# Performance work log

Hardware: AMD Instinct MI355X
Metric: run time of the kernel (lower is better)

The kernel has to match this reference:

```python
import jax, jax.numpy as jnp
import numpy as np

D_NUM = 4      # domain_num
N_ES = 2       # n_expert_specific per domain
N_SH = 4       # total shared experts (n_expert_shared_list = [1,1,1,1])
DIN = 512      # input_dims
H = 256        # expert_params dims[-1]
B = 16384      # batch
NEG_INF = -jnp.inf


def setup_inputs() -> dict:
    key = jax.random.key(0)
    ks = jax.random.split(key, 10)
    s = 1.0 / np.sqrt(DIN)
    x_list = jax.random.normal(ks[0], (D_NUM + 1, B, DIN), jnp.float32)
    sim_domain = jax.random.randint(ks[1], (D_NUM, 2), 0, D_NUM, jnp.int32)
    W_spec = jax.random.normal(ks[2], (D_NUM, N_ES, DIN, H), jnp.float32) * s
    b_spec = jax.random.normal(ks[3], (D_NUM, N_ES, H), jnp.float32) * 0.01
    W_sh = jax.random.normal(ks[4], (N_SH, DIN, H), jnp.float32) * s
    b_sh = jax.random.normal(ks[5], (N_SH, H), jnp.float32) * 0.01
    W_gate = jax.random.normal(ks[6], (D_NUM, DIN, N_ES + N_SH), jnp.float32) * s
    b_gate = jax.random.normal(ks[7], (D_NUM, N_ES + N_SH), jnp.float32) * 0.01
    W_gate_sh = jax.random.normal(ks[8], (DIN, D_NUM * N_ES + N_SH), jnp.float32) * s
    b_gate_sh = jax.random.normal(ks[9], (D_NUM * N_ES + N_SH,), jnp.float32) * 0.01
    return {"x_list": x_list, "sim_domain": sim_domain, "W_spec": W_spec,
            "b_spec": b_spec, "W_sh": W_sh, "b_sh": b_sh, "W_gate": W_gate,
            "b_gate": b_gate, "W_gate_sh": W_gate_sh, "b_gate_sh": b_gate_sh}


def reference(x_list, sim_domain, W_spec, b_spec, W_sh, b_sh, W_gate, b_gate, W_gate_sh, b_gate_sh):
    xd = x_list[:D_NUM]          # [D, B, DIN] per-domain inputs
    xs = x_list[-1]              # [B, DIN] shared input
    # expert MLPs (single hidden layer, relu, dropout=0/eval)
    spec = jax.nn.relu(jnp.einsum('nbd,nedh->nbeh', xd, W_spec) + b_spec[:, None])  # [D,B,E,H]
    shared = jax.nn.relu(jnp.einsum('bd,edh->beh', xs, W_sh) + b_sh)                # [B,S,H]
    # specific gates: softmax activation inside MLP
    g = jax.nn.softmax(jnp.einsum('nbd,nde->nbe', xd, W_gate) + b_gate[:, None], axis=-1)  # [D,B,E+S]
    # mask shared experts of non-similar domains (expert_ranges[d] = [N_ES + d])
    mem = (sim_domain[:, :, None] == jnp.arange(D_NUM)[None, None, :]).any(axis=1)  # [D,D]
    mask = jnp.concatenate([jnp.zeros((D_NUM, N_ES), jnp.float32),
                            jnp.where(mem, 0.0, NEG_INF)], axis=1)                  # [D,E+S]
    # torch code re-softmaxes the (already softmaxed) gate after adding -inf mask
    g = jax.nn.softmax(g + mask[:, None, :], axis=-1)
    # weighted combine without materializing broadcasted shared experts
    outs = (jnp.einsum('nbe,nbeh->nbh', g[..., :N_ES], spec)
            + jnp.einsum('nbe,beh->nbh', g[..., N_ES:], shared))                    # [D,B,H]
    # shared gate (cur_level < n_level)
    gs = jax.nn.softmax(xs @ W_gate_sh + b_gate_sh, axis=-1)                         # [B,D*E+S]
    all_spec = spec.transpose(1, 0, 2, 3).reshape(spec.shape[1], D_NUM * N_ES, H)    # [B,D*E,H]
    out_sh = (jnp.einsum('be,beh->bh', gs[:, :D_NUM * N_ES], all_spec)
              + jnp.einsum('be,beh->bh', gs[:, D_NUM * N_ES:], shared))             # [B,H]
    return jnp.concatenate([outs, out_sh[None]], axis=0)                             # [D+1,B,H]
```

## Files before the change

### kernel.cpp

```cpp
#include <hip/hip_runtime.h>
#include <cstdint>
#include <cstddef>

#define D_NUM 4
#define N_ES  2
#define N_SH  4
#define DIN   512
#define HDIM  256
#define BB    16384
#define MHALF 8192
#define NMAT  12
#define NGATE 36

typedef __bf16 bf16x8 __attribute__((ext_vector_type(8)));
typedef float  f32x4  __attribute__((ext_vector_type(4)));

__device__ __forceinline__ unsigned short f2bf(float f) {
    union { float f; unsigned u; } v; v.f = f;
    unsigned u = v.u;
    unsigned r = (u + 0x7FFFu + ((u >> 16) & 1u)) >> 16;
    return (unsigned short)r;
}
__device__ __forceinline__ float bf2f(unsigned short u) {
    union { unsigned u; float f; } v; v.u = ((unsigned)u) << 16; return v.f;
}
__device__ __forceinline__ void async16(void* l, const void* g) {
    __builtin_amdgcn_global_load_lds(
        (const __attribute__((address_space(1))) void*)g,
        (__attribute__((address_space(3))) void*)l,
        16, 0, 0);
}

template<int CTRL, int RMASK>
__device__ __forceinline__ float dpp_sum_step(float v) {
    union { float f; int i; } a, b;
    a.f = v;
    b.i = __builtin_amdgcn_update_dpp(0, a.i, CTRL, RMASK, 0xF, true);
    return v + b.f;
}
__device__ __forceinline__ float wave_sum63(float v) {
    v = dpp_sum_step<0x111, 0xF>(v);
    v = dpp_sum_step<0x112, 0xF>(v);
    v = dpp_sum_step<0x114, 0xF>(v);
    v = dpp_sum_step<0x118, 0xF>(v);
    v = dpp_sum_step<0x142, 0xA>(v);
    v = dpp_sum_step<0x143, 0xC>(v);
    return v;
}

__global__ __launch_bounds__(256) void k_wconv(
    const float* __restrict__ Wspec,
    const float* __restrict__ Wsh,
    unsigned short* __restrict__ WT)
{
    __shared__ unsigned short t[64][65];
    const int mat = blockIdx.z;
    const int k0  = blockIdx.x * 64;
    const int h0  = blockIdx.y * 64;
    const float* src = (mat < 8) ? (Wspec + (size_t)mat * DIN * HDIM)
                                 : (Wsh   + (size_t)(mat - 8) * DIN * HDIM);
    #pragma unroll
    for (int i = 0; i < 16; ++i) {
        int idx = i * 256 + threadIdx.x;
        int r = idx >> 6, c = idx & 63;
        t[r][c] = f2bf(src[(size_t)(k0 + r) * HDIM + h0 + c]);
    }
    __syncthreads();
    #pragma unroll
    for (int i = 0; i < 16; ++i) {
        int idx = i * 256 + threadIdx.x;
        int r = idx >> 6, c = idx & 63;
        WT[(size_t)mat * HDIM * DIN + (size_t)(h0 + r) * DIN + k0 + c] = t[c][r];
    }
}

__global__ __launch_bounds__(256) void k_gwt(
    const float* __restrict__ Wg,
    const float* __restrict__ Wgs,
    float* __restrict__ WgT,
    float* __restrict__ WgsT)
{
    int i = blockIdx.x * 256 + threadIdx.x;
    if (i < 4 * 6 * 512) {
        int n = i / 3072, rem = i % 3072;
        int e = rem >> 9, k = rem & 511;
        WgT[i] = Wg[((size_t)n * DIN + k) * 6 + e];
    }
    if (i < 12 * 512) {
        int e = i >> 9, k = i & 511;
        WgsT[i] = Wgs[(size_t)k * 12 + e];
    }
}

__global__ __launch_bounds__(128) void k_prep(
    const float* __restrict__ x,
    const int*   __restrict__ simdom,
    const float* __restrict__ WgT,
    const float* __restrict__ bg,
    const float* __restrict__ WgsT,
    const float* __restrict__ bgs,
    unsigned short* __restrict__ xbf,
    float* __restrict__ gates)
{
    __shared__ float lgate[2][2][36];
    __shared__ float gsm[2][72];
    const int wave = threadIdx.x >> 6;
    const int lane = threadIdx.x & 63;
    const int row0 = blockIdx.x * 4 + wave * 2;
    const int k0   = lane * 8;

    float4 a0[5], b0[5], a1[5], b1[5];
    #pragma unroll
    for (int m = 0; m < 5; ++m) {
        const float* xp0 = x + ((size_t)m * BB + row0) * DIN + k0;
        a0[m] = ((const float4*)xp0)[0];
        b0[m] = ((const float4*)xp0)[1];
        const float* xp1 = xp0 + DIN;
        a1[m] = ((const float4*)xp1)[0];
        b1[m] = ((const float4*)xp1)[1];
    }
    __builtin_amdgcn_sched_barrier(0);

    #pragma unroll
    for (int m = 0; m < 5; ++m) {
        unsigned short* xbp = xbf + ((size_t)m * BB + row0) * DIN + k0;
        {
            union { unsigned short us[8]; uint4 v; } q0, q1;
            q0.us[0]=f2bf(a0[m].x); q0.us[1]=f2bf(a0[m].y);
            q0.us[2]=f2bf(a0[m].z); q0.us[3]=f2bf(a0[m].w);
            q0.us[4]=f2bf(b0[m].x); q0.us[5]=f2bf(b0[m].y);
            q0.us[6]=f2bf(b0[m].z); q0.us[7]=f2bf(b0[m].w);
            q1.us[0]=f2bf(a1[m].x); q1.us[1]=f2bf(a1[m].y);
            q1.us[2]=f2bf(a1[m].z); q1.us[3]=f2bf(a1[m].w);
            q1.us[4]=f2bf(b1[m].x); q1.us[5]=f2bf(b1[m].y);
            q1.us[6]=f2bf(b1[m].z); q1.us[7]=f2bf(b1[m].w);
            *(uint4*)xbp         = q0.v;
            *(uint4*)(xbp + DIN) = q1.v;
        }
        if (m < 4) {
            float z0[6], z1[6];
            #pragma unroll
            for (int e = 0; e < 6; ++e) {
                const float* wp = WgT + ((size_t)(m * 6 + e)) * DIN + k0;
                float4 wa = ((const float4*)wp)[0], wb = ((const float4*)wp)[1];
                z0[e] = a0[m].x*wa.x + a0[m].y*wa.y + a0[m].z*wa.z + a0[m].w*wa.w
                      + b0[m].x*wb.x + b0[m].y*wb.y + b0[m].z*wb.z + b0[m].w*wb.w;
                z1[e] = a1[m].x*wa.x + a1[m].y*wa.y + a1[m].z*wa.z + a1[m].w*wa.w
                      + b1[m].x*wb.x + b1[m].y*wb.y + b1[m].z*wb.z + b1[m].w*wb.w;
            }
            #pragma unroll
            for (int e = 0; e < 6; ++e) { z0[e] = wave_sum63(z0[e]); z1[e] = wave_sum63(z1[e]); }
            if (lane == 63) {
                #pragma unroll
                for (int e = 0; e < 6; ++e) {
                    lgate[wave][0][m * 6 + e] = z0[e];
                    lgate[wave][1][m * 6 + e] = z1[e];
                }
            }
        } else {
            float z0[12], z1[12];
            #pragma unroll
            for (int e = 0; e < 12; ++e) {
                const float* wp = WgsT + (size_t)e * DIN + k0;
                float4 wa = ((const float4*)wp)[0], wb = ((const float4*)wp)[1];
                z0[e] = a0[m].x*wa.x + a0[m].y*wa.y + a0[m].z*wa.z + a0[m].w*wa.w
                      + b0[m].x*wb.x + b0[m].y*wb.y + b0[m].z*wb.z + b0[m].w*wb.w;
                z1[e] = a1[m].x*wa.x + a1[m].y*wa.y + a1[m].z*wa.z + a1[m].w*wa.w
                      + b1[m].x*wb.x + b1[m].y*wb.y + b1[m].z*wb.z + b1[m].w*wb.w;
            }
            #pragma unroll
            for (int e = 0; e < 12; ++e) { z0[e] = wave_sum63(z0[e]); z1[e] = wave_sum63(z1[e]); }
            if (lane == 63) {
                #pragma unroll
                for (int e = 0; e < 12; ++e) {
                    lgate[wave][0][24 + e] = z0[e];
                    lgate[wave][1][24 + e] = z1[e];
                }
            }
        }
    }
    asm volatile("s_waitcnt lgkmcnt(0)" ::: "memory");
    __builtin_amdgcn_wave_barrier();

    if (lane < 2) {
        const float* lg = lgate[wave][lane];
        float*       go = &gsm[wave][lane * 36];
        #pragma unroll
        for (int n = 0; n < 4; ++n) {
            float z[6];
            #pragma unroll
            for (int e = 0; e < 6; ++e) z[e] = lg[n * 6 + e] + bg[n * 6 + e];
            float mx = z[0];
            #pragma unroll
            for (int e = 1; e < 6; ++e) mx = fmaxf(mx, z[e]);
            float sum = 0.f;
            #pragma unroll
            for (int e = 0; e < 6; ++e) { z[e] = __expf(z[e] - mx); sum += z[e]; }
            float inv = 1.f / sum;
            #pragma unroll
            for (int e = 0; e < 6; ++e) z[e] *= inv;
            int s0 = simdom[n * 2], s1 = simdom[n * 2 + 1];
            float w[6];
            w[0] = z[0]; w[1] = z[1];
            #pragma unroll
            for (int j = 0; j < 4; ++j)
                w[2 + j] = (s0 == j || s1 == j) ? z[2 + j] : -1e30f;
            float mx2 = w[0];
            #pragma unroll
            for (int e = 1; e < 6; ++e) mx2 = fmaxf(mx2, w[e]);
            float sm = 0.f;
            #pragma unroll
            for (int e = 0; e < 6; ++e) { w[e] = __expf(w[e] - mx2); sm += w[e]; }
            float iv = 1.f / sm;
            #pragma unroll
            for (int e = 0; e < 6; ++e) go[n * 6 + e] = w[e] * iv;
        }
        {
            float z[12];
            #pragma unroll
            for (int e = 0; e < 12; ++e) z[e] = lg[24 + e] + bgs[e];
            float mx = z[0];
            #pragma unroll
            for (int e = 1; e < 12; ++e) mx = fmaxf(mx, z[e]);
            float sum = 0.f;
            #pragma unroll
            for (int e = 0; e < 12; ++e) { z[e] = __expf(z[e] - mx); sum += z[e]; }
            float inv = 1.f / sum;
            #pragma unroll
            for (int e = 0; e < 12; ++e) go[24 + e] = z[e] * inv;
        }
    }
    __builtin_amdgcn_wave_barrier();
    for (int j = lane; j < 72; j += 64)
        gates[(size_t)row0 * NGATE + j] = gsm[wave][j];
}

__global__ __launch_bounds__(256) void k_gemm(
    const unsigned short* __restrict__ xbf,
    const unsigned short* __restrict__ WT,
    const float* __restrict__ bspec,
    const float* __restrict__ bsh,
    unsigned short* __restrict__ S,
    int row_base)
{
    __shared__ unsigned short lbuf[17408];

    const int tid  = threadIdx.x;
    const int wave = tid >> 6;
    const int lane = tid & 63;

    const int j    = blockIdx.x + 24 * blockIdx.y;
    const int xcd  = j & 7;
    const int slot = j >> 3;
    const int rg   = xcd * 8 + slot / 24;
    const int mh   = slot % 24;

    const int mat  = mh >> 1;
    const int hh0  = (mh & 1) * 128;
    const int plane = (mat < 8) ? (mat >> 1) : 4;
    const int lrow0 = rg * 128;

    const unsigned short* Abase = xbf + ((size_t)plane * BB + row_base + lrow0) * DIN;
    const unsigned short* Bbase = WT + (size_t)mat * HDIM * DIN + (size_t)hh0 * DIN;

    const unsigned short* gb = (wave < 2) ? Abase : Bbase;
    unsigned goff[8];
    unsigned loff[8];
    {
        int cg = (lane & 7) ^ ((lane >> 3) & 7);
        #pragma unroll
        for (int i = 0; i < 8; ++i) {
            int slot2 = wave * 8 + i;
            int r = (slot2 & 15) * 8 + (lane >> 3);
            goff[i] = (unsigned)(r * DIN + cg * 8);
            loff[i] = (unsigned)(slot2 * 512);
        }
    }

    f32x4 acc[4][4];
    #pragma unroll
    for (int t = 0; t < 4; ++t)
        #pragma unroll
        for (int u = 0; u < 4; ++u)
            acc[t][u] = (f32x4){0.f, 0.f, 0.f, 0.f};

    const int wm = wave >> 1, wn = wave & 1;
    const int arow = lane & 15, quad = lane >> 4;
    int aofs[4], bofs[4];
    #pragma unroll
    for (int t = 0; t < 4; ++t) {
        int r = wm * 64 + t * 16 + arow;
        aofs[t] = r * 64 + (quad ^ (r & 7)) * 8;
    }
    #pragma unroll
    for (int u = 0; u < 4; ++u) {
        int r = wn * 64 + u * 16 + arow;
        bofs[u] = 8192 + r * 64 + (quad ^ (r & 7)) * 8;
    }

    for (int ks = 0; ks < 8; ++ks) {
        __syncthreads();
        #pragma unroll
        for (int i = 0; i < 8; ++i) {
            async16(lbuf + loff[i], gb + goff[i]);
            goff[i] += 64;
        }
        __syncthreads();

        #pragma unroll
        for (int s2 = 0; s2 < 2; ++s2) {
            const int sx = s2 * 32;
            bf16x8 af[4], bv[4];
            #pragma unroll
            for (int t = 0; t < 4; ++t) af[t] = *(const bf16x8*)(lbuf + (aofs[t] ^ sx));
            #pragma unroll
            for (int u = 0; u < 4; ++u) bv[u] = *(const bf16x8*)(lbuf + (bofs[u] ^ sx));
            #pragma unroll
            for (int t = 0; t < 4; ++t)
                #pragma unroll
                for (int u = 0; u < 4; ++u)
                    acc[t][u] = __builtin_amdgcn_mfma_f32_16x16x32_bf16(af[t], bv[u], acc[t][u], 0, 0, 0);
        }
    }

    __syncthreads();
    #pragma unroll
    for (int u = 0; u < 4; ++u) {
        const int hc = wn * 64 + u * 16 + arow;
        const float bias = (mat < 8) ? bspec[mat * HDIM + hh0 + hc]
                                     : bsh[(mat - 8) * HDIM + hh0 + hc];
        #pragma unroll
        for (int t = 0; t < 4; ++t) {
            const int rbase = wm * 64 + t * 16 + quad * 4;
            #pragma unroll
            for (int reg = 0; reg < 4; ++reg) {
                float v = fmaxf(acc[t][u][reg] + bias, 0.f);
                lbuf[(rbase + reg) * 136 + hc] = f2bf(v);
            }
        }
    }
    __syncthreads();
    {
        unsigned short* Sb = S + ((size_t)mat * MHALF + lrow0) * HDIM + hh0;
        #pragma unroll
        for (int i = 0; i < 8; ++i) {
            int idx = i * 256 + tid;
            int row = idx >> 4, c8 = idx & 15;
            *(uint4*)(Sb + (size_t)row * HDIM + c8 * 8) =
                *(const uint4*)(lbuf + row * 136 + c8 * 8);
        }
    }
}

__global__ __launch_bounds__(256) void k_comb(
    const unsigned short* __restrict__ S,
    const float* __restrict__ gates,
    float* __restrict__ out,
    int row_base)
{
    const int tid = threadIdx.x;
    const int h0  = (tid & 63) * 4;
    const int r0  = blockIdx.x * 8 + (tid >> 6) * 2;
    #pragma unroll
    for (int rr = 0; rr < 2; ++rr) {
        const int lr = r0 + rr;
        const int grow = row_base + lr;
        const float* g = gates + (size_t)grow * NGATE;
        float s[NMAT][4];
        #pragma unroll
        for (int mat = 0; mat < NMAT; ++mat) {
            uint2 u = *(const uint2*)(S + ((size_t)mat * MHALF + lr) * HDIM + h0);
            s[mat][0] = bf2f((unsigned short)(u.x & 0xFFFFu));
            s[mat][1] = bf2f((unsigned short)(u.x >> 16));
            s[mat][2] = bf2f((unsigned short)(u.y & 0xFFFFu));
            s[mat][3] = bf2f((unsigned short)(u.y >> 16));
        }
        float o4[4] = {0.f, 0.f, 0.f, 0.f};
        #pragma unroll
        for (int jj = 0; jj < 8; ++jj)
            #pragma unroll
            for (int c = 0; c < 4; ++c) o4[c] += g[24 + jj] * s[jj][c];
        #pragma unroll
        for (int e = 0; e < 4; ++e)
            #pragma unroll
            for (int c = 0; c < 4; ++c) o4[c] += g[32 + e] * s[8 + e][c];
        #pragma unroll
        for (int n = 0; n < 4; ++n) {
            float4 on;
            on.x = g[n*6+0]*s[n*2][0] + g[n*6+1]*s[n*2+1][0]
                 + g[n*6+2]*s[8][0] + g[n*6+3]*s[9][0] + g[n*6+4]*s[10][0] + g[n*6+5]*s[11][0];
            on.y = g[n*6+0]*s[n*2][1] + g[n*6+1]*s[n*2+1][1]
                 + g[n*6+2]*s[8][1] + g[n*6+3]*s[9][1] + g[n*6+4]*s[10][1] + g[n*6+5]*s[11][1];
            on.z = g[n*6+0]*s[n*2][2] + g[n*6+1]*s[n*2+1][2]
                 + g[n*6+2]*s[8][2] + g[n*6+3]*s[9][2] + g[n*6+4]*s[10][2] + g[n*6+5]*s[11][2];
            on.w = g[n*6+0]*s[n*2][3] + g[n*6+1]*s[n*2+1][3]
                 + g[n*6+2]*s[8][3] + g[n*6+3]*s[9][3] + g[n*6+4]*s[10][3] + g[n*6+5]*s[11][3];
            *(float4*)(out + ((size_t)n * BB + grow) * HDIM + h0) = on;
        }
        float4 o4v = {o4[0], o4[1], o4[2], o4[3]};
        *(float4*)(out + ((size_t)4 * BB + grow) * HDIM + h0) = o4v;
    }
}

extern "C" void kernel_launch(void* const* d_in, const int* in_sizes, int n_in,
                              void* d_out, int out_size, void* d_ws, size_t ws_size,
                              hipStream_t stream) {
    const float* x      = (const float*)d_in[0];
    const int*   simdom = (const int*)  d_in[1];
    const float* Wspec  = (const float*)d_in[2];
    const float* bspec  = (const float*)d_in[3];
    const float* Wsh    = (const float*)d_in[4];
    const float* bsh    = (const float*)d_in[5];
    const float* Wg     = (const float*)d_in[6];
    const float* bg     = (const float*)d_in[7];
    const float* Wgs    = (const float*)d_in[8];
    const float* bgs    = (const float*)d_in[9];
    float* out = (float*)d_out;

    uint8_t* ws = (uint8_t*)d_ws;
    unsigned short* xbf  = (unsigned short*)(ws);
    unsigned short* WT   = (unsigned short*)(ws + 83886080ull);
    float*          gts  = (float*)(ws + 87031808ull);
    float*          WgT  = (float*)(ws + 89391104ull);
    float*          WgsT = (float*)(ws + 89440256ull);
    unsigned short* S    = (unsigned short*)(ws + 89464832ull);

    k_wconv<<<dim3(8, 4, 12), 256, 0, stream>>>(Wspec, Wsh, WT);
    k_gwt<<<48, 256, 0, stream>>>(Wg, Wgs, WgT, WgsT);
    k_prep<<<BB / 4, 128, 0, stream>>>(x, simdom, WgT, bg, WgsT, bgs, xbf, gts);
    for (int half = 0; half < 2; ++half) {
        int row_base = half * MHALF;
        k_gemm<<<dim3(24, 64), 256, 0, stream>>>(xbf, WT, bspec, bsh, S, row_base);
        k_comb<<<MHALF / 8, 256, 0, stream>>>(S, gts, out, row_base);
    }
}
```

Measured before the change: 397.2 us.

## Double-buffer LDS tiles in expert GEMM to overlap loads with MFMA

The GEMM kernel now ping-pongs two LDS buffers, issuing the async global-to-LDS copy for the next K-slice before computing on the current one, with explicit vmcnt waits and raw s_barriers in place of __syncthreads pairs. Bias values are loaded once before the main loop rather than in the epilogue. The aim is to hide global load latency behind the matrix instructions. In exchange LDS per block roughly doubles (64KB), which may lower occupancy, and the hand-written waitcnt/barrier ordering is fragile.

```diff
diff --git a/kernel.cpp b/kernel.cpp
--- a/kernel.cpp
+++ b/kernel.cpp
@@ -243,7 +243,7 @@
     unsigned short* __restrict__ S,
     int row_base)
 {
-    __shared__ unsigned short lbuf[17408];
+    __shared__ unsigned short lbuf[32768];
 
     const int tid  = threadIdx.x;
     const int wave = tid >> 6;
@@ -277,13 +277,6 @@
         }
     }
 
-    f32x4 acc[4][4];
-    #pragma unroll
-    for (int t = 0; t < 4; ++t)
-        #pragma unroll
-        for (int u = 0; u < 4; ++u)
-            acc[t][u] = (f32x4){0.f, 0.f, 0.f, 0.f};
-
     const int wm = wave >> 1, wn = wave & 1;
     const int arow = lane & 15, quad = lane >> 4;
     int aofs[4], bofs[4];
@@ -298,43 +291,76 @@
         bofs[u] = 8192 + r * 64 + (quad ^ (r & 7)) * 8;
     }
 
+    float bias[4];
+    #pragma unroll
+    for (int u = 0; u < 4; ++u) {
+        const int hc = wn * 64 + u * 16 + arow;
+        bias[u] = (mat < 8) ? bspec[mat * HDIM + hh0 + hc]
+                            : bsh[(mat - 8) * HDIM + hh0 + hc];
+    }
+    asm volatile("s_waitcnt vmcnt(0)" ::: "memory");
+    __builtin_amdgcn_sched_barrier(0);
+
+    f32x4 acc[4][4];
+    #pragma unroll
+    for (int t = 0; t < 4; ++t)
+        #pragma unroll
+        for (int u = 0; u < 4; ++u)
+            acc[t][u] = (f32x4){0.f, 0.f, 0.f, 0.f};
+
+    #pragma unroll
+    for (int i = 0; i < 8; ++i) {
+        async16(lbuf + loff[i], gb + goff[i]);
+        goff[i] += 64;
+    }
+
+    int cur = 0;
     for (int ks = 0; ks < 8; ++ks) {
-        __syncthreads();
-        #pragma unroll
-        for (int i = 0; i < 8; ++i) {
-            async16(lbuf + loff[i], gb + goff[i]);
-            goff[i] += 64;
-        }
-        __syncthreads();
-
+        if (ks < 7) {
+            unsigned short* nb = lbuf + (cur ^ 1) * 16384;
+            #pragma unroll
+            for (int i = 0; i < 8; ++i) {
+                async16(nb + loff[i], gb + goff[i]);
+                goff[i] += 64;
+            }
+            asm volatile("s_waitcnt vmcnt(8)" ::: "memory");
+        } else {
+            asm volatile("s_waitcnt vmcnt(0)" ::: "memory");
+        }
+        __builtin_amdgcn_sched_barrier(0);
+        __builtin_amdgcn_s_barrier();
+        __builtin_amdgcn_sched_barrier(0);
+
+        const unsigned short* bb = lbuf + cur * 16384;
         #pragma unroll
         for (int s2 = 0; s2 < 2; ++s2) {
             const int sx = s2 * 32;
             bf16x8 af[4], bv[4];
             #pragma unroll
-            for (int t = 0; t < 4; ++t) af[t] = *(const bf16x8*)(lbuf + (aofs[t] ^ sx));
-            #pragma unroll
-            for (int u = 0; u < 4; ++u) bv[u] = *(const bf16x8*)(lbuf + (bofs[u] ^ sx));
+            for (int t = 0; t < 4; ++t) af[t] = *(const bf16x8*)(bb + (aofs[t] ^ sx));
+            #pragma unroll
+            for (int u = 0; u < 4; ++u) bv[u] = *(const bf16x8*)(bb + (bofs[u] ^ sx));
             #pragma unroll
             for (int t = 0; t < 4; ++t)
                 #pragma unroll
                 for (int u = 0; u < 4; ++u)
                     acc[t][u] = __builtin_amdgcn_mfma_f32_16x16x32_bf16(af[t], bv[u], acc[t][u], 0, 0, 0);
         }
-    }
-
-    __syncthreads();
+        __builtin_amdgcn_sched_barrier(0);
+        __builtin_amdgcn_s_barrier();
+        __builtin_amdgcn_sched_barrier(0);
+        cur ^= 1;
+    }
+
     #pragma unroll
     for (int u = 0; u < 4; ++u) {
         const int hc = wn * 64 + u * 16 + arow;
-        const float bias = (mat < 8) ? bspec[mat * HDIM + hh0 + hc]
-                                     : bsh[(mat - 8) * HDIM + hh0 + hc];
         #pragma unroll
         for (int t = 0; t < 4; ++t) {
             const int rbase = wm * 64 + t * 16 + quad * 4;
             #pragma unroll
             for (int reg = 0; reg < 4; ++reg) {
-                float v = fmaxf(acc[t][u][reg] + bias, 0.f);
+                float v = fmaxf(acc[t][u][reg] + bias[u], 0.f);
                 lbuf[(rbase + reg) * 136 + hc] = f2bf(v);
             }
         }
```

Result: no change. 403.3 us (+1.5%).
